# Kernel tuning notes

Measured on AMD Instinct MI355X. Metric: run time of the kernel, lower is better.

Reference implementation:

```python
import jax, jax.numpy as jnp
import numpy as np

N = 131072      # total nodes
B = 512         # number of graphs
F_DIM = 512     # in_channels
H = F_DIM // 2  # score_net hidden
RATIO = 0.5
MARGIN = 0.5
TOPK_LOSS_WEIGHT = 0.2


def setup_inputs() -> dict:
    key = jax.random.key(0)
    k1, k2, k3 = jax.random.split(key, 3)
    x = jax.random.normal(k1, (N, F_DIM), dtype=jnp.float32)
    # sorted segment ids: equal-sized graphs of N // B nodes
    batch = (jnp.arange(N) // (N // B)).astype(jnp.int32)
    W1 = jax.random.normal(k2, (F_DIM, H), dtype=jnp.float32) / np.sqrt(F_DIM).astype(np.float32)
    b1 = jnp.zeros((H,), dtype=jnp.float32)
    W2 = jax.random.normal(k3, (H, 1), dtype=jnp.float32) / np.sqrt(H).astype(np.float32)
    b2 = jnp.zeros((1,), dtype=jnp.float32)
    return {"x": x, "batch": batch, "W1": W1, "b1": b1, "W2": W2, "b2": b2}


def reference(x, batch, W1, b1, W2, b2):
    # scores = score_net(x).squeeze(-1)   [N]
    scores = (jax.nn.relu(x @ W1 + b1) @ W2 + b2)[:, 0]

    # per-graph node counts and k = max(1, int(ratio * n_i))
    counts = jax.ops.segment_sum(jnp.ones((N,), dtype=scores.dtype), batch, num_segments=B)
    k = jnp.maximum(1, jnp.floor(RATIO * counts).astype(jnp.int32))  # [B]

    # segmented top-k via lexsort: sort by (batch asc, score desc)
    order = jnp.lexsort((-scores, batch))          # [N] permutation
    b_sorted = batch[order]
    starts = jnp.cumsum(counts) - counts           # exclusive-cumsum segment starts
    rank = jnp.arange(N, dtype=counts.dtype) - starts[b_sorted]  # rank within graph (0 = highest score)
    sel_sorted = rank < k[b_sorted].astype(counts.dtype)
    selected_mask = jnp.zeros((N,), dtype=bool).at[order].set(sel_sorted)

    # global_add_pool over selected nodes
    m = selected_mask.astype(x.dtype)
    x_pooled = jax.ops.segment_sum(x * m[:, None], batch, num_segments=B)  # [B, F]

    # margin regularization loss per graph
    sel_cnt = jax.ops.segment_sum(m, batch, num_segments=B)
    sel_sum = jax.ops.segment_sum(scores * m, batch, num_segments=B)
    tot_sum = jax.ops.segment_sum(scores, batch, num_segments=B)
    uns_cnt = counts - sel_cnt
    sel_mean = sel_sum / jnp.maximum(sel_cnt, 1.0)
    uns_mean = (tot_sum - sel_sum) / jnp.maximum(uns_cnt, 1.0)
    per_graph = jnp.where(uns_cnt > 0, jax.nn.relu(MARGIN - (sel_mean - uns_mean)), 0.0)
    topk_loss = per_graph.sum() / B * TOPK_LOSS_WEIGHT

    return x_pooled, topk_loss, selected_mask
```

## Files before the change

kernel.cpp:

```cpp
#include <hip/hip_runtime.h>

#define N_NODES 131072
#define BGRAPHS 512
#define FDIM    512
#define HDIM    256
#define NPG     256
#define KSEL    128
#define STAGES  16
#define STAGE_UNITS 3072
#define STAGE_BYTES (STAGE_UNITS * 16)

typedef __attribute__((ext_vector_type(8)))  short bf16x8;
typedef __attribute__((ext_vector_type(16))) float f32x16;

__device__ __forceinline__ unsigned short bf16_rne(float f, float* back) {
    unsigned u = __float_as_uint(f);
    unsigned r = u + 0x7FFFu + ((u >> 16) & 1u);
    unsigned short h = (unsigned short)(r >> 16);
    *back = __uint_as_float(((unsigned)h) << 16);
    return h;
}

__global__ __launch_bounds__(256)
void split_w1_kernel(const float* __restrict__ W1, unsigned short* __restrict__ wsB)
{
    const int uid  = blockIdx.x * 256 + threadIdx.x;
    const int lane = uid & 63;
    int t = uid >> 6;
    const int nt = t & 7;  t >>= 3;
    const int q  = t & 1;  t >>= 1;
    const int p  = t % 3;
    const int s  = t / 3;
    const int n  = nt * 32 + (lane & 31);
    const int k0 = s * 32 + q * 16 + (lane >> 5) * 8;

    bf16x8 v;
    #pragma unroll
    for (int j = 0; j < 8; ++j) {
        float w = W1[(size_t)(k0 + j) * HDIM + n];
        float f1, f2, f3;
        unsigned short h1 = bf16_rne(w, &f1);
        float r1 = w - f1;
        unsigned short h2 = bf16_rne(r1, &f2);
        float r2 = r1 - f2;
        unsigned short h3 = bf16_rne(r2, &f3);
        v[j] = (short)(p == 0 ? h1 : (p == 1 ? h2 : h3));
    }
    *(bf16x8*)(wsB + (size_t)uid * 8) = v;
}

__global__ __launch_bounds__(256, 2)
void score_mfma_kernel(const float* __restrict__ x,
                       const unsigned short* __restrict__ wsB,
                       const float* __restrict__ b1, const float* __restrict__ W2,
                       const float* __restrict__ b2, float* __restrict__ scores)
{
    __shared__ unsigned short ldsB[STAGE_BYTES / 2];
    __shared__ float Sp[2][128];

    const int tid  = threadIdx.x;
    const int lane = tid & 63;
    const int wv   = tid >> 6;
    const int wy   = wv & 1;
    const int wx   = wv >> 1;
    const int l31  = lane & 31;
    const int lh   = lane >> 5;
    const int m_base = blockIdx.x * 128 + wy * 64;

    f32x16 acc[2][4];
    #pragma unroll
    for (int a = 0; a < 2; ++a)
        #pragma unroll
        for (int b = 0; b < 4; ++b)
            #pragma unroll
            for (int r = 0; r < 16; ++r) acc[a][b][r] = 0.f;

    for (int s = 0; s < STAGES; ++s) {
        __syncthreads();
        const unsigned short* src = wsB + (size_t)s * (STAGE_BYTES / 2);
        #pragma unroll
        for (int i = 0; i < 12; ++i) {
            const int unit = i * 256 + tid;
            __builtin_amdgcn_global_load_lds(
                (const __attribute__((address_space(1))) unsigned int*)(src + (size_t)unit * 8),
                (__attribute__((address_space(3))) unsigned int*)(ldsB + unit * 8),
                16, 0, 0);
        }
        __syncthreads();

        #pragma unroll
        for (int q = 0; q < 2; ++q) {
            float4 xa[2], xb[2];
            #pragma unroll
            for (int mt = 0; mt < 2; ++mt) {
                const int row = m_base + mt * 32 + l31;
                const float* xp = x + (size_t)row * FDIM + s * 32 + q * 16 + lh * 8;
                xa[mt] = *(const float4*)xp;
                xb[mt] = *(const float4*)(xp + 4);
            }
            const bf16x8* bfp = (const bf16x8*)ldsB;
            bf16x8 Bh[4], Bm[4], Bl[4];
            #pragma unroll
            for (int nt = 0; nt < 4; ++nt) {
                const int nn = wx * 4 + nt;
                Bh[nt] = bfp[((0 * 2 + q) * 8 + nn) * 64 + lane];
                Bm[nt] = bfp[((1 * 2 + q) * 8 + nn) * 64 + lane];
                Bl[nt] = bfp[((2 * 2 + q) * 8 + nn) * 64 + lane];
            }
            #pragma unroll
            for (int mt = 0; mt < 2; ++mt) {
                float v[8] = {xa[mt].x, xa[mt].y, xa[mt].z, xa[mt].w,
                              xb[mt].x, xb[mt].y, xb[mt].z, xb[mt].w};
                bf16x8 Ah, Am, Al;
                #pragma unroll
                for (int j = 0; j < 8; ++j) {
                    float f1, f2, f3;
                    unsigned short h1 = bf16_rne(v[j], &f1);
                    float r1 = v[j] - f1;
                    unsigned short h2 = bf16_rne(r1, &f2);
                    float r2 = r1 - f2;
                    unsigned short h3 = bf16_rne(r2, &f3);
                    Ah[j] = (short)h1; Am[j] = (short)h2; Al[j] = (short)h3;
                }
                #pragma unroll
                for (int nt = 0; nt < 4; ++nt) {
                    acc[mt][nt] = __builtin_amdgcn_mfma_f32_32x32x16_bf16(Ah, Bh[nt], acc[mt][nt], 0, 0, 0);
                    acc[mt][nt] = __builtin_amdgcn_mfma_f32_32x32x16_bf16(Ah, Bm[nt], acc[mt][nt], 0, 0, 0);
                    acc[mt][nt] = __builtin_amdgcn_mfma_f32_32x32x16_bf16(Am, Bh[nt], acc[mt][nt], 0, 0, 0);
                    acc[mt][nt] = __builtin_amdgcn_mfma_f32_32x32x16_bf16(Ah, Bl[nt], acc[mt][nt], 0, 0, 0);
                    acc[mt][nt] = __builtin_amdgcn_mfma_f32_32x32x16_bf16(Al, Bh[nt], acc[mt][nt], 0, 0, 0);
                    acc[mt][nt] = __builtin_amdgcn_mfma_f32_32x32x16_bf16(Am, Bm[nt], acc[mt][nt], 0, 0, 0);
                }
            }
        }
    }

    float bb[4], ww[4];
    #pragma unroll
    for (int nt = 0; nt < 4; ++nt) {
        const int c = wx * 128 + nt * 32 + l31;
        bb[nt] = b1[c];
        ww[nt] = W2[c];
    }
    #pragma unroll
    for (int mt = 0; mt < 2; ++mt) {
        float pr[16];
        #pragma unroll
        for (int r = 0; r < 16; ++r) pr[r] = 0.f;
        #pragma unroll
        for (int nt = 0; nt < 4; ++nt)
            #pragma unroll
            for (int r = 0; r < 16; ++r) {
                float h = acc[mt][nt][r] + bb[nt];
                h = h > 0.f ? h : 0.f;
                pr[r] = fmaf(h, ww[nt], pr[r]);
            }
        #pragma unroll
        for (int mask = 1; mask <= 16; mask <<= 1)
            #pragma unroll
            for (int r = 0; r < 16; ++r)
                pr[r] += __shfl_xor(pr[r], mask);
        if (l31 == 0) {
            #pragma unroll
            for (int r = 0; r < 16; ++r) {
                const int row = wy * 64 + mt * 32 + (r & 3) + 8 * (r >> 2) + 4 * lh;
                Sp[wx][row] = pr[r];
            }
        }
    }
    __syncthreads();
    if (tid < 128)
        scores[blockIdx.x * 128 + tid] = b2[0] + Sp[0][tid] + Sp[1][tid];
}

__global__ __launch_bounds__(256)
void select_kernel(const float* __restrict__ scores, float* __restrict__ mask_out,
                   int* __restrict__ sel_idx, float* __restrict__ loss_per_g)
{
    __shared__ float s[NPG];
    __shared__ float redT[NPG];
    __shared__ float redS[NPG];
    const int g = blockIdx.x;
    const int t = threadIdx.x;

    const float sc = scores[g * NPG + t];
    s[t] = sc;
    __syncthreads();

    int rank = 0;
    for (int j = 0; j < NPG; ++j) {
        const float sj = s[j];
        rank += (sj > sc || (sj == sc && j < t)) ? 1 : 0;
    }
    const bool sel = rank < KSEL;
    mask_out[g * NPG + t] = sel ? 1.0f : 0.0f;
    if (sel) sel_idx[g * KSEL + rank] = t;

    redT[t] = sc;
    redS[t] = sel ? sc : 0.f;
    __syncthreads();
    for (int off = 128; off > 0; off >>= 1) {
        if (t < off) { redT[t] += redT[t + off]; redS[t] += redS[t + off]; }
        __syncthreads();
    }
    if (t == 0) {
        const float tot = redT[0], ssum = redS[0];
        const float sel_mean = ssum * (1.0f / KSEL);
        const float uns_mean = (tot - ssum) * (1.0f / (NPG - KSEL));
        const float v = 0.5f - (sel_mean - uns_mean);
        loss_per_g[g] = v > 0.f ? v : 0.f;
    }
}

__global__ __launch_bounds__(256)
void pool_kernel(const float* __restrict__ x, const int* __restrict__ sel_idx,
                 float* __restrict__ pooled)
{
    const int b    = blockIdx.x;
    const int g    = b >> 1;
    const int half = b & 1;
    const int t    = threadIdx.x;
    const int col  = half * 256 + t;

    __shared__ int idx[KSEL];
    if (t < KSEL) idx[t] = sel_idx[g * KSEL + t];
    __syncthreads();

    const float* __restrict__ xg = x + (size_t)g * NPG * FDIM;
    float a0 = 0.f, a1 = 0.f, a2 = 0.f, a3 = 0.f;
    #pragma unroll 4
    for (int n = 0; n < KSEL; n += 4) {
        a0 += xg[(size_t)idx[n + 0] * FDIM + col];
        a1 += xg[(size_t)idx[n + 1] * FDIM + col];
        a2 += xg[(size_t)idx[n + 2] * FDIM + col];
        a3 += xg[(size_t)idx[n + 3] * FDIM + col];
    }
    pooled[g * FDIM + col] = (a0 + a1) + (a2 + a3);
}

__global__ __launch_bounds__(256)
void loss_kernel(const float* __restrict__ loss_per_g, float* __restrict__ out_loss)
{
    __shared__ float red[256];
    const int t = threadIdx.x;
    red[t] = loss_per_g[t] + loss_per_g[t + 256];
    __syncthreads();
    for (int off = 128; off > 0; off >>= 1) {
        if (t < off) red[t] += red[t + off];
        __syncthreads();
    }
    if (t == 0) out_loss[0] = red[0] * (0.2f / BGRAPHS);
}

extern "C" void kernel_launch(void* const* d_in, const int* in_sizes, int n_in,
                              void* d_out, int out_size, void* d_ws, size_t ws_size,
                              hipStream_t stream)
{
    const float* x  = (const float*)d_in[0];
    const float* W1 = (const float*)d_in[2];
    const float* b1 = (const float*)d_in[3];
    const float* W2 = (const float*)d_in[4];
    const float* b2 = (const float*)d_in[5];

    float* out    = (float*)d_out;
    float* pooled = out;
    float* loss   = out + BGRAPHS * FDIM;
    float* mask   = loss + 1;

    float* scores  = (float*)d_ws;
    int*   sel_idx = (int*)((char*)d_ws + 524288);
    float* loss_g  = (float*)((char*)d_ws + 786432);
    unsigned short* wsB = (unsigned short*)((char*)d_ws + 1048576);

    split_w1_kernel<<<192, 256, 0, stream>>>(W1, wsB);
    score_mfma_kernel<<<N_NODES / 128, 256, 0, stream>>>(x, wsB, b1, W2, b2, scores);
    select_kernel<<<BGRAPHS, 256, 0, stream>>>(scores, mask, sel_idx, loss_g);
    pool_kernel<<<BGRAPHS * 2, 256, 0, stream>>>(x, sel_idx, pooled);
    loss_kernel<<<1, 256, 0, stream>>>(loss_g, loss);
}
```

Before: 497.3 us.

## Fuse score GEMM, top-k selection and pooling into one per-graph kernel

Merges the score MFMA kernel, the selection kernel and the pooling kernel into one kernel where each 512-thread block handles a whole graph of 256 nodes. Scores and selected indices stay in shared memory instead of round-tripping through global workspace, and two kernel launches are removed. Pooling re-reads the graph's x rows right after the GEMM streamed them, which may hit in cache. In exchange there are only 512 blocks, each with larger shared memory and register use, so occupancy and load balance could suffer, and the selection phase leaves half the threads idle.

New measurement: 1.940 ms. 290% more time.

```diff
diff --git a/kernel.cpp b/kernel.cpp
--- a/kernel.cpp
+++ b/kernel.cpp
@@ -49,23 +49,30 @@
     *(bf16x8*)(wsB + (size_t)uid * 8) = v;
 }
 
-__global__ __launch_bounds__(256, 2)
-void score_mfma_kernel(const float* __restrict__ x,
-                       const unsigned short* __restrict__ wsB,
-                       const float* __restrict__ b1, const float* __restrict__ W2,
-                       const float* __restrict__ b2, float* __restrict__ scores)
+__global__ __launch_bounds__(512, 4)
+void fused_kernel(const float* __restrict__ x,
+                  const unsigned short* __restrict__ wsB,
+                  const float* __restrict__ b1, const float* __restrict__ W2,
+                  const float* __restrict__ b2,
+                  float* __restrict__ pooled, float* __restrict__ mask_out,
+                  float* __restrict__ loss_per_g)
 {
     __shared__ unsigned short ldsB[STAGE_BYTES / 2];
-    __shared__ float Sp[2][128];
-
+    __shared__ float Sp[2][NPG];
+    __shared__ float sv[NPG];
+    __shared__ int   selr[KSEL];
+    __shared__ float redT[NPG];
+    __shared__ float redS[NPG];
+
+    const int g    = blockIdx.x;
     const int tid  = threadIdx.x;
     const int lane = tid & 63;
     const int wv   = tid >> 6;
-    const int wy   = wv & 1;
-    const int wx   = wv >> 1;
+    const int wy   = wv & 3;
+    const int wx   = wv >> 2;
     const int l31  = lane & 31;
     const int lh   = lane >> 5;
-    const int m_base = blockIdx.x * 128 + wy * 64;
+    const int m_base = g * NPG + wy * 64;
 
     f32x16 acc[2][4];
     #pragma unroll
@@ -79,8 +86,8 @@
         __syncthreads();
         const unsigned short* src = wsB + (size_t)s * (STAGE_BYTES / 2);
         #pragma unroll
-        for (int i = 0; i < 12; ++i) {
-            const int unit = i * 256 + tid;
+        for (int i = 0; i < 6; ++i) {
+            const int unit = i * 512 + tid;
             __builtin_amdgcn_global_load_lds(
                 (const __attribute__((address_space(1))) unsigned int*)(src + (size_t)unit * 8),
                 (__attribute__((address_space(3))) unsigned int*)(ldsB + unit * 8),
@@ -169,71 +176,50 @@
         }
     }
     __syncthreads();
-    if (tid < 128)
-        scores[blockIdx.x * 128 + tid] = b2[0] + Sp[0][tid] + Sp[1][tid];
-}
-
-__global__ __launch_bounds__(256)
-void select_kernel(const float* __restrict__ scores, float* __restrict__ mask_out,
-                   int* __restrict__ sel_idx, float* __restrict__ loss_per_g)
-{
-    __shared__ float s[NPG];
-    __shared__ float redT[NPG];
-    __shared__ float redS[NPG];
-    const int g = blockIdx.x;
-    const int t = threadIdx.x;
-
-    const float sc = scores[g * NPG + t];
-    s[t] = sc;
-    __syncthreads();
-
-    int rank = 0;
-    for (int j = 0; j < NPG; ++j) {
-        const float sj = s[j];
-        rank += (sj > sc || (sj == sc && j < t)) ? 1 : 0;
-    }
-    const bool sel = rank < KSEL;
-    mask_out[g * NPG + t] = sel ? 1.0f : 0.0f;
-    if (sel) sel_idx[g * KSEL + rank] = t;
-
-    redT[t] = sc;
-    redS[t] = sel ? sc : 0.f;
-    __syncthreads();
+
+    float sc = 0.f;
+    if (tid < NPG) {
+        sc = b2[0] + Sp[0][tid] + Sp[1][tid];
+        sv[tid] = sc;
+    }
+    __syncthreads();
+
+    bool sel = false;
+    if (tid < NPG) {
+        int rank = 0;
+        for (int j = 0; j < NPG; ++j) {
+            const float sj = sv[j];
+            rank += (sj > sc || (sj == sc && j < tid)) ? 1 : 0;
+        }
+        sel = rank < KSEL;
+        mask_out[g * NPG + tid] = sel ? 1.0f : 0.0f;
+        if (sel) selr[rank] = tid;
+        redT[tid] = sc;
+        redS[tid] = sel ? sc : 0.f;
+    }
+    __syncthreads();
+
     for (int off = 128; off > 0; off >>= 1) {
-        if (t < off) { redT[t] += redT[t + off]; redS[t] += redS[t + off]; }
-        __syncthreads();
-    }
-    if (t == 0) {
+        if (tid < off) { redT[tid] += redT[tid + off]; redS[tid] += redS[tid + off]; }
+        __syncthreads();
+    }
+    if (tid == 0) {
         const float tot = redT[0], ssum = redS[0];
         const float sel_mean = ssum * (1.0f / KSEL);
         const float uns_mean = (tot - ssum) * (1.0f / (NPG - KSEL));
         const float v = 0.5f - (sel_mean - uns_mean);
         loss_per_g[g] = v > 0.f ? v : 0.f;
     }
-}
-
-__global__ __launch_bounds__(256)
-void pool_kernel(const float* __restrict__ x, const int* __restrict__ sel_idx,
-                 float* __restrict__ pooled)
-{
-    const int b    = blockIdx.x;
-    const int g    = b >> 1;
-    const int half = b & 1;
-    const int t    = threadIdx.x;
-    const int col  = half * 256 + t;
-
-    __shared__ int idx[KSEL];
-    if (t < KSEL) idx[t] = sel_idx[g * KSEL + t];
-    __syncthreads();
-
+
+    const int col = tid;
     const float* __restrict__ xg = x + (size_t)g * NPG * FDIM;
     float a0 = 0.f, a1 = 0.f, a2 = 0.f, a3 = 0.f;
     #pragma unroll 4
     for (int n = 0; n < KSEL; n += 4) {
-        a0 += xg[(size_t)idx[n + 0] * FDIM + col];
-        a1 += xg[(size_t)idx[n + 1] * FDIM + col];
-        a2 += xg[(size_t)idx[n + 2] * FDIM + col];
-        a3 += xg[(size_t)idx[n + 3] * FDIM + col];
+        a0 += xg[(size_t)selr[n + 0] * FDIM + col];
+        a1 += xg[(size_t)selr[n + 1] * FDIM + col];
+        a2 += xg[(size_t)selr[n + 2] * FDIM + col];
+        a3 += xg[(size_t)selr[n + 3] * FDIM + col];
     }
     pooled[g * FDIM + col] = (a0 + a1) + (a2 + a3);
 }
@@ -267,14 +253,11 @@
     float* loss   = out + BGRAPHS * FDIM;
     float* mask   = loss + 1;
 
-    float* scores  = (float*)d_ws;
-    int*   sel_idx = (int*)((char*)d_ws + 524288);
-    float* loss_g  = (float*)((char*)d_ws + 786432);
-    unsigned short* wsB = (unsigned short*)((char*)d_ws + 1048576);
+    float* loss_g       = (float*)d_ws;
+    unsigned short* wsB = (unsigned short*)((char*)d_ws + 4096);
 
     split_w1_kernel<<<192, 256, 0, stream>>>(W1, wsB);
-    score_mfma_kernel<<<N_NODES / 128, 256, 0, stream>>>(x, wsB, b1, W2, b2, scores);
-    select_kernel<<<BGRAPHS, 256, 0, stream>>>(scores, mask, sel_idx, loss_g);
-    pool_kernel<<<BGRAPHS * 2, 256, 0, stream>>>(x, sel_idx, pooled);
+    fused_kernel<<<BGRAPHS, 512, 0, stream>>>(x, wsB, b1, W2, b2,
+                                              pooled, mask, loss_g);
     loss_kernel<<<1, 256, 0, stream>>>(loss_g, loss);
 }
```
